# Kernel tuning notes

Hardware: AMD Instinct MI355X
Metric: run time of the kernel (lower is better)

Reference implementation:

```python
import jax, jax.numpy as jnp
import numpy as np

K = 7  # local_kernel_size


def conv2d(x, w, b, pad):
    # x: [B,C,H,W], w: [O,I,kh,kw]
    y = jax.lax.conv_general_dilated(
        x, w, window_strides=(1, 1), padding=[(pad, pad), (pad, pad)],
        dimension_numbers=("NCHW", "OIHW", "NCHW"))
    return y + b[None, :, None, None]


def kernel_normalize(kernel, k):
    # kernel: [B, k*k, H, W]; zero-mean over tap dim, then add 1/(k*k)
    km = jnp.mean(kernel, axis=1, keepdims=True)
    return kernel - km + 1.0 / (k * k)


def local_conv_feat(img, kernel, k):
    # Fused dynamic local conv: avoids materializing [B,C,k*k,H,W].
    # Tap order matches F.unfold row-major (dy, dx).
    B, C, H, W = img.shape
    pad = (k - 1) // 2
    imgp = jnp.pad(img, ((0, 0), (0, 0), (pad, pad), (pad, pad)))
    out = jnp.zeros_like(img)
    for dy in range(k):
        for dx in range(k):
            idx = dy * k + dx
            out = out + imgp[:, :, dy:dy + H, dx:dx + W] * kernel[:, idx:idx + 1]
    return out


def setup_inputs() -> dict:
    key = jax.random.key(0)
    ks = jax.random.split(key, 14)
    B, C, H, W = 4, 64, 128, 128
    w = lambda k, shape: jax.random.normal(k, shape, jnp.float32) * 0.05
    return {
        "x": jax.random.normal(ks[0], (B, C, H, W), jnp.float32),
        "kernel_features": jax.random.normal(ks[1], (B, C, H, W), jnp.float32),
        # feature_path: two 3x3 convs
        "fw1": w(ks[2], (C, C, 3, 3)), "fb1": jnp.zeros((C,), jnp.float32),
        "fw2": w(ks[3], (C, C, 3, 3)), "fb2": jnp.zeros((C,), jnp.float32),
        # multiplicative_path: two 3x3 convs
        "mw1": w(ks[4], (C, C, 3, 3)), "mb1": jnp.zeros((C,), jnp.float32),
        "mw2": w(ks[5], (C, C, 3, 3)), "mb2": jnp.zeros((C,), jnp.float32),
        # local_filter_path: two 1x1 convs, last outputs k*k channels
        "lw1": w(ks[6], (C, C, 1, 1)), "lb1": jnp.zeros((C,), jnp.float32),
        "lw2": w(ks[7], (K * K, C, 1, 1)), "lb2": jnp.zeros((K * K,), jnp.float32),
    }


def reference(x, kernel_features, fw1, fb1, fw2, fb2, mw1, mb1, mw2, mb2, lw1, lb1, lw2, lb2):
    # feature_path: ReLU -> conv3x3 -> ReLU -> conv3x3
    fp = conv2d(jax.nn.relu(conv2d(jax.nn.relu(x), fw1, fb1, 1)), fw2, fb2, 1)
    # multiplicative_path: conv3x3 -> ReLU -> conv3x3
    mp = conv2d(jax.nn.relu(conv2d(kernel_features, mw1, mb1, 1)), mw2, mb2, 1)
    # local_filter_path: conv1x1 -> ReLU -> conv1x1 (-> k*k channels)
    lp = conv2d(jax.nn.relu(conv2d(kernel_features, lw1, lb1, 0)), lw2, lb2, 0)
    lp = kernel_normalize(lp, K)
    feat = fp * mp
    filtered = local_conv_feat(feat, lp, K)
    return x + filtered
```

## Files before the change

kernel.cpp:

```cpp
#include <hip/hip_runtime.h>
#include <hip/hip_bf16.h>

#define Cc 64
#define Hc 128
#define Wc 128
#define HWc (Hc * Wc)
#define Bc 4

typedef __attribute__((ext_vector_type(8))) short short8;
typedef __attribute__((ext_vector_type(4))) float float4v;

static __device__ __forceinline__ unsigned short f2bu(float f) {
    __hip_bfloat16 h = __float2bfloat16(f);
    return *(unsigned short*)&h;
}

__global__ __launch_bounds__(256) void cvt_both_k(
    const float* __restrict__ x, const float* __restrict__ kf,
    unsigned short* __restrict__ xb, unsigned short* __restrict__ kfb)
{
    const int bid = blockIdx.x;
    const bool isx = bid < 256;
    const float* src = isx ? x : kf;
    unsigned short* dst = isx ? xb : kfb;
    const int px = (isx ? bid : bid - 256) * 256 + threadIdx.x;
    const int b  = px >> 14;
    const int hw = px & 16383;
    const float* s = src + (size_t)b * Cc * HWc + hw;
    unsigned short* d = dst + (size_t)px * Cc;

#pragma unroll
    for (int c8 = 0; c8 < 8; ++c8) {
        unsigned int pk[4];
#pragma unroll
        for (int jp = 0; jp < 4; ++jp) {
            float v0 = s[(size_t)(c8 * 8 + jp * 2 + 0) * HWc];
            float v1 = s[(size_t)(c8 * 8 + jp * 2 + 1) * HWc];
            if (isx) { v0 = fmaxf(v0, 0.f); v1 = fmaxf(v1, 0.f); }
            pk[jp] = (unsigned int)f2bu(v0) | ((unsigned int)f2bu(v1) << 16);
        }
        *(uint4*)(d + c8 * 8) = make_uint4(pk[0], pk[1], pk[2], pk[3]);
    }
}

__global__ __launch_bounds__(256) void wpack_all_k(
    const float* __restrict__ fw1, const float* __restrict__ fw2,
    const float* __restrict__ mw1, const float* __restrict__ mw2,
    const float* __restrict__ lw1, const float* __restrict__ lw2,
    unsigned short* __restrict__ wbase)
{
    const int bid = blockIdx.x;
    const int tid = threadIdx.x;
    if (bid < 72) {
        const int which = bid / 18;
        const float* w = (which == 0) ? fw1 : (which == 1) ? fw2 : (which == 2) ? mw1 : mw2;
        unsigned short* wb = wbase + (size_t)which * 36864;
        const int g = (bid % 18) * 256 + tid;
        if (g >= 4608) return;
        const int lane = g & 63;
        const int smt  = g >> 6;
        const int s    = smt >> 2;
        const int mt   = smt & 3;
        const int co   = mt * 16 + (lane & 15);
        const int kb   = s * 32 + (lane >> 4) * 8;
        unsigned int pk[4];
#pragma unroll
        for (int jp = 0; jp < 4; ++jp) {
            int k0 = kb + jp * 2, k1 = k0 + 1;
            float v0 = w[((size_t)co * Cc + (k0 & 63)) * 9 + (k0 >> 6)];
            float v1 = w[((size_t)co * Cc + (k1 & 63)) * 9 + (k1 >> 6)];
            pk[jp] = (unsigned int)f2bu(v0) | ((unsigned int)f2bu(v1) << 16);
        }
        *(uint4*)(wb + (size_t)g * 8) = make_uint4(pk[0], pk[1], pk[2], pk[3]);
    } else {
        const int which = (bid - 72) >> 1;
        const float* w = which ? lw2 : lw1;
        const int Cout = which ? 49 : 64;
        unsigned short* wb = wbase + 4 * 36864 + (size_t)which * 4096;
        const int g = ((bid - 72) & 1) * 256 + tid;
        const int lane = g & 63;
        const int smt  = g >> 6;
        const int s    = smt >> 2;
        const int mt   = smt & 3;
        const int co   = mt * 16 + (lane & 15);
        const int kb   = s * 32 + (lane >> 4) * 8;
        unsigned int pk[4];
#pragma unroll
        for (int jp = 0; jp < 4; ++jp) {
            int k0 = kb + jp * 2, k1 = k0 + 1;
            float v0 = (co < Cout) ? w[(size_t)co * Cc + k0] : 0.f;
            float v1 = (co < Cout) ? w[(size_t)co * Cc + k1] : 0.f;
            pk[jp] = (unsigned int)f2bu(v0) | ((unsigned int)f2bu(v1) << 16);
        }
        *(uint4*)(wb + (size_t)g * 8) = make_uint4(pk[0], pk[1], pk[2], pk[3]);
    }
}

template <bool RELU_OUT, bool MUL, bool F32_NCHW_OUT, bool DUAL>
__global__ __launch_bounds__(256) void conv3x3_v4(
    const unsigned short* __restrict__ in0,
    const unsigned short* __restrict__ in1,
    const unsigned short* __restrict__ wfrag0,
    const unsigned short* __restrict__ wfrag1,
    const float* __restrict__ bias0,
    const float* __restrict__ bias1,
    const unsigned short* __restrict__ fp_mul,
    void* __restrict__ out0, void* __restrict__ out1)
{
    __shared__ unsigned short s_b[264 * 64];

    const int tid  = threadIdx.x;
    const int lane = tid & 63;
    const int wv   = tid >> 6;
    const int w0   = blockIdx.x * 64;
    const int h0   = blockIdx.y * 2;
    const int zz   = blockIdx.z;
    const int b    = DUAL ? (zz & 3) : zz;
    const bool sel = DUAL ? (zz >> 2) : 0;

    const unsigned short* in    = sel ? in1 : in0;
    const unsigned short* wfrag = sel ? wfrag1 : wfrag0;
    const float*          bias  = sel ? bias1 : bias0;
    void*                 out   = sel ? out1 : out0;

    for (int u = tid; u < 264; u += 256) {
        const int r  = u / 66;
        const int c  = u - r * 66;
        const int gh = h0 - 1 + r;
        const int gw = w0 - 1 + c;
        const bool ok = ((unsigned)gh < (unsigned)Hc) && ((unsigned)gw < (unsigned)Wc);
        const unsigned short* src =
            in + (((size_t)b * Hc + (ok ? gh : 0)) * Wc + (ok ? gw : 0)) * Cc;
        const int sw = u & 7;
#pragma unroll
        for (int ch = 0; ch < 8; ++ch) {
            uint4 v = ok ? *(const uint4*)(src + ch * 8) : make_uint4(0, 0, 0, 0);
            *(uint4*)&s_b[u * 64 + ((ch ^ sw) << 3)] = v;
        }
    }
    __syncthreads();

    const int rowsel = wv >> 1;
    const int cohalf = wv & 1;
    const int quad   = lane >> 4;
    const int n15    = lane & 15;

    const unsigned short* aptr = wfrag + (((size_t)(cohalf * 2) * 64 + lane) << 3);

    int rowb[3];
#pragma unroll
    for (int ky = 0; ky < 3; ++ky) rowb[ky] = (rowsel + ky) * 66 + n15;

    float4v acc[2][4];
#pragma unroll
    for (int m = 0; m < 2; ++m)
#pragma unroll
        for (int nt = 0; nt < 4; ++nt) acc[m][nt] = (float4v){0.f, 0.f, 0.f, 0.f};

#define LOAD_A(s, m) (*(const short8*)(aptr + (size_t)(s) * 2048 + (size_t)(m) * 512))
#define LOAD_B(s, nt) ({                                                     \
        const int tap_ = (s) >> 1;                                           \
        const int qb_  = rowb[tap_ / 3] + tap_ % 3;                          \
        const int ch0_ = ((s) & 1) * 4 + quad;                               \
        *(const short8*)&s_b[(qb_ + (nt) * 16) * 64 + ((ch0_ ^ (qb_ & 7)) << 3)]; })

    short8 a_cur[2], b_cur[4];
#pragma unroll
    for (int m = 0; m < 2; ++m) a_cur[m] = LOAD_A(0, m);
#pragma unroll
    for (int nt = 0; nt < 4; ++nt) b_cur[nt] = LOAD_B(0, nt);

#pragma unroll
    for (int s = 0; s < 18; ++s) {
        short8 a_nxt[2], b_nxt[4];
        if (s < 17) {
#pragma unroll
            for (int m = 0; m < 2; ++m) a_nxt[m] = LOAD_A(s + 1, m);
#pragma unroll
            for (int nt = 0; nt < 4; ++nt) b_nxt[nt] = LOAD_B(s + 1, nt);
        }
#pragma unroll
        for (int nt = 0; nt < 4; ++nt)
#pragma unroll
            for (int m = 0; m < 2; ++m)
                acc[m][nt] = __builtin_amdgcn_mfma_f32_16x16x32_bf16(
                    a_cur[m], b_cur[nt], acc[m][nt], 0, 0, 0);
        if (s < 17) {
#pragma unroll
            for (int m = 0; m < 2; ++m) a_cur[m] = a_nxt[m];
#pragma unroll
            for (int nt = 0; nt < 4; ++nt) b_cur[nt] = b_nxt[nt];
        }
    }
#undef LOAD_A
#undef LOAD_B

    const int h = h0 + rowsel;
#pragma unroll
    for (int m = 0; m < 2; ++m) {
        const int mt  = cohalf * 2 + m;
        const int co0 = mt * 16 + quad * 4;
        float4 bv = *(const float4*)&bias[co0];
#pragma unroll
        for (int nt = 0; nt < 4; ++nt) {
            const size_t pix = ((size_t)b * Hc + h) * Wc + w0 + nt * 16 + n15;
            float v[4] = {acc[m][nt][0] + bv.x, acc[m][nt][1] + bv.y,
                          acc[m][nt][2] + bv.z, acc[m][nt][3] + bv.w};
            if (RELU_OUT)
#pragma unroll
                for (int r = 0; r < 4; ++r) v[r] = fmaxf(v[r], 0.f);
            if (MUL) {
                uint2 mm = *(const uint2*)&fp_mul[pix * Cc + co0];
                v[0] *= __uint_as_float((mm.x & 0xffffu) << 16);
                v[1] *= __uint_as_float(mm.x & 0xffff0000u);
                v[2] *= __uint_as_float((mm.y & 0xffffu) << 16);
                v[3] *= __uint_as_float(mm.y & 0xffff0000u);
            }
            if (F32_NCHW_OUT) {
                float* op = (float*)out;
#pragma unroll
                for (int r = 0; r < 4; ++r)
                    op[((size_t)b * Cc + co0 + r) * HWc + (size_t)h * Wc + w0 + nt * 16 + n15] = v[r];
            } else {
                unsigned short* op = (unsigned short*)out;
                ushort4 pk;
                pk.x = f2bu(v[0]); pk.y = f2bu(v[1]); pk.z = f2bu(v[2]); pk.w = f2bu(v[3]);
                *(ushort4*)&op[pix * Cc + co0] = pk;
            }
        }
    }
}

__global__ __launch_bounds__(256) void lp_fused_k(
    const unsigned short* __restrict__ in,
    const unsigned short* __restrict__ w1,
    const float* __restrict__ b1,
    const unsigned short* __restrict__ w2,
    const float* __restrict__ b2,
    float* __restrict__ out)
{
    __shared__ unsigned short s_t[4 * 1024];

    const int tid  = threadIdx.x;
    const int lane = tid & 63;
    const int wv   = tid >> 6;
    const int quad = lane >> 4;
    const int p    = lane & 15;
    const size_t pix = (size_t)blockIdx.x * 64 + wv * 16 + p;
    unsigned short* st = &s_t[wv * 1024];

    float4v acc1[4];
#pragma unroll
    for (int mt = 0; mt < 4; ++mt) acc1[mt] = (float4v){0.f, 0.f, 0.f, 0.f};
#pragma unroll
    for (int s = 0; s < 2; ++s) {
        short8 bfr = *(const short8*)&in[pix * Cc + s * 32 + quad * 8];
#pragma unroll
        for (int mt = 0; mt < 4; ++mt) {
            short8 afr = *(const short8*)&w1[(size_t)(((s * 4 + mt) << 6) + lane) << 3];
            acc1[mt] = __builtin_amdgcn_mfma_f32_16x16x32_bf16(afr, bfr, acc1[mt], 0, 0, 0);
        }
    }

#pragma unroll
    for (int mt = 0; mt < 4; ++mt) {
        const int co0 = mt * 16 + quad * 4;
        float4 bv = *(const float4*)&b1[co0];
        ushort4 pk;
        pk.x = f2bu(fmaxf(acc1[mt][0] + bv.x, 0.f));
        pk.y = f2bu(fmaxf(acc1[mt][1] + bv.y, 0.f));
        pk.z = f2bu(fmaxf(acc1[mt][2] + bv.z, 0.f));
        pk.w = f2bu(fmaxf(acc1[mt][3] + bv.w, 0.f));
        const int cg = co0 >> 3;
        *(ushort4*)&st[p * 64 + ((cg ^ (p & 7)) << 3) + (quad & 1) * 4] = pk;
    }
    __syncthreads();

    float4v acc2[4];
#pragma unroll
    for (int mt = 0; mt < 4; ++mt) acc2[mt] = (float4v){0.f, 0.f, 0.f, 0.f};
#pragma unroll
    for (int s = 0; s < 2; ++s) {
        const int cg = s * 4 + quad;
        short8 bfr = *(const short8*)&st[p * 64 + ((cg ^ (p & 7)) << 3)];
#pragma unroll
        for (int mt = 0; mt < 4; ++mt) {
            short8 afr = *(const short8*)&w2[(size_t)(((s * 4 + mt) << 6) + lane) << 3];
            acc2[mt] = __builtin_amdgcn_mfma_f32_16x16x32_bf16(afr, bfr, acc2[mt], 0, 0, 0);
        }
    }

    float v[4][4];
    float partial = 0.f;
#pragma unroll
    for (int mt = 0; mt < 4; ++mt) {
#pragma unroll
        for (int r = 0; r < 4; ++r) {
            const int tap = mt * 16 + quad * 4 + r;
            float val = (tap < 49) ? (acc2[mt][r] + b2[tap]) : 0.f;
            v[mt][r] = val;
            partial += val;
        }
    }
    partial += __shfl_xor(partial, 16, 64);
    partial += __shfl_xor(partial, 32, 64);
    const float m = partial * (1.f / 49.f) - (1.f / 49.f);

    const int b  = (int)(pix >> 14);
    const int hw = (int)(pix & 16383);
#pragma unroll
    for (int mt = 0; mt < 4; ++mt) {
#pragma unroll
        for (int r = 0; r < 4; ++r) {
            const int tap = mt * 16 + quad * 4 + r;
            if (tap < 49)
                out[((size_t)b * 49 + tap) * HWc + hw] = v[mt][r] - m;
        }
    }
}

__global__ __launch_bounds__(256) void local_conv_v2(
    const float* __restrict__ x, const float* __restrict__ feat,
    const float* __restrict__ lp, float* __restrict__ out)
{
    const int tid = threadIdx.x;
    const int w4  = (tid & 31) * 4;
    const int ro  = tid >> 5;
    const int h   = blockIdx.x * 8 + ro;
    const int c0  = blockIdx.y * 4;
    const int b   = blockIdx.z;

    float msk[12];
#pragma unroll
    for (int e = 0; e < 12; ++e) {
        int gw = w4 - 4 + e;
        msk[e] = ((unsigned)gw < (unsigned)Wc) ? 1.f : 0.f;
    }

    float acc[4][4];
#pragma unroll
    for (int ch = 0; ch < 4; ++ch)
#pragma unroll
        for (int p = 0; p < 4; ++p) acc[ch][p] = 0.f;

    const float* lpb = lp + (size_t)b * 49 * HWc + (size_t)h * Wc + w4;
    const float* fb  = feat + ((size_t)b * Cc + c0) * HWc;

#pragma unroll
    for (int dy = 0; dy < 7; ++dy) {
        const int gh = h + dy - 3;
        if ((unsigned)gh >= (unsigned)Hc) continue;

        float4 lp4[7];
#pragma unroll
        for (int dx = 0; dx < 7; ++dx)
            lp4[dx] = *(const float4*)&lpb[(size_t)(dy * 7 + dx) * HWc];

        const float* frow = fb + (size_t)gh * Wc + w4;
#pragma unroll
        for (int ch = 0; ch < 4; ++ch) {
            const float* fr = frow + (size_t)ch * HWc;
            float4 a  = *(const float4*)(fr - 4);
            float4 bq = *(const float4*)(fr);
            float4 cq = *(const float4*)(fr + 4);
            float f[12];
            f[0]  = a.x;            f[1]  = a.y * msk[1];
            f[2]  = a.z * msk[2];   f[3]  = a.w * msk[3];
            f[4]  = bq.x;           f[5]  = bq.y;
            f[6]  = bq.z;           f[7]  = bq.w;
            f[8]  = cq.x * msk[8];  f[9]  = cq.y * msk[9];
            f[10] = cq.z * msk[10]; f[11] = cq.w;
#pragma unroll
            for (int dx = 0; dx < 7; ++dx) {
                const float* lpv = (const float*)&lp4[dx];
#pragma unroll
                for (int p = 0; p < 4; ++p)
                    acc[ch][p] = fmaf(f[p + dx + 1], lpv[p], acc[ch][p]);
            }
        }
    }

#pragma unroll
    for (int ch = 0; ch < 4; ++ch) {
        const size_t idx = ((size_t)b * Cc + c0 + ch) * HWc + (size_t)h * Wc + w4;
        float4 xv = *(const float4*)&x[idx];
        float4 r  = {acc[ch][0] + xv.x, acc[ch][1] + xv.y,
                     acc[ch][2] + xv.z, acc[ch][3] + xv.w};
        *(float4*)&out[idx] = r;
    }
}

extern "C" void kernel_launch(void* const* d_in, const int* in_sizes, int n_in,
                              void* d_out, int out_size, void* d_ws, size_t ws_size,
                              hipStream_t stream)
{
    const float* x   = (const float*)d_in[0];
    const float* kf  = (const float*)d_in[1];
    const float* fw1 = (const float*)d_in[2];
    const float* fb1 = (const float*)d_in[3];
    const float* fw2 = (const float*)d_in[4];
    const float* fb2 = (const float*)d_in[5];
    const float* mw1 = (const float*)d_in[6];
    const float* mb1 = (const float*)d_in[7];
    const float* mw2 = (const float*)d_in[8];
    const float* mb2 = (const float*)d_in[9];
    const float* lw1 = (const float*)d_in[10];
    const float* lb1 = (const float*)d_in[11];
    const float* lw2 = (const float*)d_in[12];
    const float* lb2 = (const float*)d_in[13];

    float* out = (float*)d_out;
    char*  ws  = (char*)d_ws;

    const size_t NBH = (size_t)Bc * HWc * Cc * 2;
    const size_t NBF = (size_t)Bc * Cc * HWc * 4;
    const size_t LPB = (size_t)Bc * 49 * HWc * 4;

    unsigned short* t1f   = (unsigned short*)(ws);
    unsigned short* t1m   = (unsigned short*)(ws + NBH);
    float*          feat  = (float*)(ws + 2 * NBH);
    float*          lpb   = (float*)(ws + 2 * NBH + NBF);
    unsigned short* xb    = (unsigned short*)(ws + 2 * NBH + NBF + LPB);
    unsigned short* kfb   = (unsigned short*)((char*)xb + NBH);
    unsigned short* wbase = (unsigned short*)((char*)kfb + NBH);
    unsigned short* wb1   = wbase;
    unsigned short* wb2   = wbase + 36864;
    unsigned short* wb3   = wbase + 2 * 36864;
    unsigned short* wb4   = wbase + 3 * 36864;
    unsigned short* wl1   = wbase + 4 * 36864;
    unsigned short* wl2   = wbase + 4 * 36864 + 4096;
    unsigned short* fp    = (unsigned short*)d_out;

    dim3 blk(256);
    dim3 gm (Wc / 64, Hc / 2, Bc);
    dim3 gm2(Wc / 64, Hc / 2, Bc * 2);
    dim3 gp (Bc * HWc / 64);
    dim3 glc(Hc / 8, Cc / 4, Bc);

    cvt_both_k<<<dim3(512), blk, 0, stream>>>(x, kf, xb, kfb);
    wpack_all_k<<<dim3(76), blk, 0, stream>>>(fw1, fw2, mw1, mw2, lw1, lw2, wbase);

    conv3x3_v4<true, false, false, true><<<gm2, blk, 0, stream>>>(
        xb, kfb, wb1, wb3, fb1, mb1, nullptr, t1f, t1m);

    conv3x3_v4<false, false, false, false><<<gm, blk, 0, stream>>>(
        t1f, nullptr, wb2, nullptr, fb2, nullptr, nullptr, fp, nullptr);

    conv3x3_v4<false, true, true, false><<<gm, blk, 0, stream>>>(
        t1m, nullptr, wb4, nullptr, mb2, nullptr, fp, feat, nullptr);

    lp_fused_k<<<gp, blk, 0, stream>>>(kfb, wl1, lb1, wl2, lb2, lpb);

    local_conv_v2<<<glc, blk, 0, stream>>>(x, feat, lpb, out);
}
```

Before: 194.1 us.

## Fuse second-stage convs and fold local filter path into local conv

Merges the feature and multiplicative second 3x3 convs into one kernel that keeps the feature result in registers and multiplies before writing feat. Also computes the 1x1 local-filter path per 16x4 tile inside the local conv kernel, holding normalized taps in shared memory instead of a full fp32 buffer. This removes global round trips for fp and the 49-tap filter tensor and two launches, at the cost of fewer concurrent conv blocks and smaller local-conv tiles with more halo reloads of feat.

After: 203.0 us. 1.05x slower.

```diff
diff --git a/kernel.cpp b/kernel.cpp
--- a/kernel.cpp
+++ b/kernel.cpp
@@ -96,16 +96,70 @@
     }
 }
 
-template <bool RELU_OUT, bool MUL, bool F32_NCHW_OUT, bool DUAL>
-__global__ __launch_bounds__(256) void conv3x3_v4(
+#define STAGE_TILE(INPTR)                                                     \
+    for (int u = tid; u < 264; u += 256) {                                    \
+        const int r_  = u / 66;                                               \
+        const int c_  = u - r_ * 66;                                          \
+        const int gh_ = h0 - 1 + r_;                                          \
+        const int gw_ = w0 - 1 + c_;                                          \
+        const bool ok_ = ((unsigned)gh_ < (unsigned)Hc) && ((unsigned)gw_ < (unsigned)Wc); \
+        const unsigned short* src_ =                                          \
+            (INPTR) + (((size_t)b * Hc + (ok_ ? gh_ : 0)) * Wc + (ok_ ? gw_ : 0)) * Cc; \
+        const int sw_ = u & 7;                                                \
+        _Pragma("unroll")                                                     \
+        for (int ch_ = 0; ch_ < 8; ++ch_) {                                   \
+            uint4 v_ = ok_ ? *(const uint4*)(src_ + ch_ * 8) : make_uint4(0, 0, 0, 0); \
+            *(uint4*)&s_b[u * 64 + ((ch_ ^ sw_) << 3)] = v_;                  \
+        }                                                                     \
+    }
+
+#define LOAD_A(W, s, m) (*(const short8*)((W) + (size_t)(s) * 2048 + (size_t)(m) * 512))
+#define LOAD_B(s, nt) ({                                                      \
+        const int tap_ = (s) >> 1;                                            \
+        const int qb_  = rowb[tap_ / 3] + tap_ % 3;                           \
+        const int ch0_ = ((s) & 1) * 4 + quad;                                \
+        *(const short8*)&s_b[(qb_ + (nt) * 16) * 64 + ((ch0_ ^ (qb_ & 7)) << 3)]; })
+
+#define CONV_GEMM(APTR, ACC)                                                  \
+    {                                                                         \
+        short8 a_cur[2], b_cur[4];                                            \
+        _Pragma("unroll")                                                     \
+        for (int m = 0; m < 2; ++m) a_cur[m] = LOAD_A(APTR, 0, m);            \
+        _Pragma("unroll")                                                     \
+        for (int nt = 0; nt < 4; ++nt) b_cur[nt] = LOAD_B(0, nt);             \
+        _Pragma("unroll")                                                     \
+        for (int s = 0; s < 18; ++s) {                                        \
+            short8 a_nxt[2], b_nxt[4];                                        \
+            if (s < 17) {                                                     \
+                _Pragma("unroll")                                             \
+                for (int m = 0; m < 2; ++m) a_nxt[m] = LOAD_A(APTR, s + 1, m);\
+                _Pragma("unroll")                                             \
+                for (int nt = 0; nt < 4; ++nt) b_nxt[nt] = LOAD_B(s + 1, nt); \
+            }                                                                 \
+            _Pragma("unroll")                                                 \
+            for (int nt = 0; nt < 4; ++nt)                                    \
+                _Pragma("unroll")                                             \
+                for (int m = 0; m < 2; ++m)                                   \
+                    ACC[m][nt] = __builtin_amdgcn_mfma_f32_16x16x32_bf16(     \
+                        a_cur[m], b_cur[nt], ACC[m][nt], 0, 0, 0);            \
+            if (s < 17) {                                                     \
+                _Pragma("unroll")                                             \
+                for (int m = 0; m < 2; ++m) a_cur[m] = a_nxt[m];              \
+                _Pragma("unroll")                                             \
+                for (int nt = 0; nt < 4; ++nt) b_cur[nt] = b_nxt[nt];         \
+            }                                                                 \
+        }                                                                     \
+    }
+
+__global__ __launch_bounds__(256) void conv1_dual_k(
     const unsigned short* __restrict__ in0,
     const unsigned short* __restrict__ in1,
     const unsigned short* __restrict__ wfrag0,
     const unsigned short* __restrict__ wfrag1,
     const float* __restrict__ bias0,
     const float* __restrict__ bias1,
-    const unsigned short* __restrict__ fp_mul,
-    void* __restrict__ out0, void* __restrict__ out1)
+    unsigned short* __restrict__ out0,
+    unsigned short* __restrict__ out1)
 {
     __shared__ unsigned short s_b[264 * 64];
 
@@ -115,36 +169,21 @@
     const int w0   = blockIdx.x * 64;
     const int h0   = blockIdx.y * 2;
     const int zz   = blockIdx.z;
-    const int b    = DUAL ? (zz & 3) : zz;
-    const bool sel = DUAL ? (zz >> 2) : 0;
+    const int b    = zz & 3;
+    const bool sel = zz >> 2;
 
     const unsigned short* in    = sel ? in1 : in0;
     const unsigned short* wfrag = sel ? wfrag1 : wfrag0;
     const float*          bias  = sel ? bias1 : bias0;
-    void*                 out   = sel ? out1 : out0;
-
-    for (int u = tid; u < 264; u += 256) {
-        const int r  = u / 66;
-        const int c  = u - r * 66;
-        const int gh = h0 - 1 + r;
-        const int gw = w0 - 1 + c;
-        const bool ok = ((unsigned)gh < (unsigned)Hc) && ((unsigned)gw < (unsigned)Wc);
-        const unsigned short* src =
-            in + (((size_t)b * Hc + (ok ? gh : 0)) * Wc + (ok ? gw : 0)) * Cc;
-        const int sw = u & 7;
-#pragma unroll
-        for (int ch = 0; ch < 8; ++ch) {
-            uint4 v = ok ? *(const uint4*)(src + ch * 8) : make_uint4(0, 0, 0, 0);
-            *(uint4*)&s_b[u * 64 + ((ch ^ sw) << 3)] = v;
-        }
-    }
+    unsigned short*       out   = sel ? out1 : out0;
+
+    STAGE_TILE(in);
     __syncthreads();
 
     const int rowsel = wv >> 1;
     const int cohalf = wv & 1;
     const int quad   = lane >> 4;
     const int n15    = lane & 15;
-
     const unsigned short* aptr = wfrag + (((size_t)(cohalf * 2) * 64 + lane) << 3);
 
     int rowb[3];
@@ -157,43 +196,7 @@
 #pragma unroll
         for (int nt = 0; nt < 4; ++nt) acc[m][nt] = (float4v){0.f, 0.f, 0.f, 0.f};
 
-#define LOAD_A(s, m) (*(const short8*)(aptr + (size_t)(s) * 2048 + (size_t)(m) * 512))
-#define LOAD_B(s, nt) ({                                                     \
-        const int tap_ = (s) >> 1;                                           \
-        const int qb_  = rowb[tap_ / 3] + tap_ % 3;                          \
-        const int ch0_ = ((s) & 1) * 4 + quad;                               \
-        *(const short8*)&s_b[(qb_ + (nt) * 16) * 64 + ((ch0_ ^ (qb_ & 7)) << 3)]; })
-
-    short8 a_cur[2], b_cur[4];
-#pragma unroll
-    for (int m = 0; m < 2; ++m) a_cur[m] = LOAD_A(0, m);
-#pragma unroll
-    for (int nt = 0; nt < 4; ++nt) b_cur[nt] = LOAD_B(0, nt);
-
-#pragma unroll
-    for (int s = 0; s < 18; ++s) {
-        short8 a_nxt[2], b_nxt[4];
-        if (s < 17) {
-#pragma unroll
-            for (int m = 0; m < 2; ++m) a_nxt[m] = LOAD_A(s + 1, m);
-#pragma unroll
-            for (int nt = 0; nt < 4; ++nt) b_nxt[nt] = LOAD_B(s + 1, nt);
-        }
-#pragma unroll
-        for (int nt = 0; nt < 4; ++nt)
-#pragma unroll
-            for (int m = 0; m < 2; ++m)
-                acc[m][nt] = __builtin_amdgcn_mfma_f32_16x16x32_bf16(
-                    a_cur[m], b_cur[nt], acc[m][nt], 0, 0, 0);
-        if (s < 17) {
-#pragma unroll
-            for (int m = 0; m < 2; ++m) a_cur[m] = a_nxt[m];
-#pragma unroll
-            for (int nt = 0; nt < 4; ++nt) b_cur[nt] = b_nxt[nt];
-        }
-    }
-#undef LOAD_A
-#undef LOAD_B
+    CONV_GEMM(aptr, acc);
 
     const int h = h0 + rowsel;
 #pragma unroll
@@ -204,41 +207,116 @@
 #pragma unroll
         for (int nt = 0; nt < 4; ++nt) {
             const size_t pix = ((size_t)b * Hc + h) * Wc + w0 + nt * 16 + n15;
+            ushort4 pk;
+            pk.x = f2bu(fmaxf(acc[m][nt][0] + bv.x, 0.f));
+            pk.y = f2bu(fmaxf(acc[m][nt][1] + bv.y, 0.f));
+            pk.z = f2bu(fmaxf(acc[m][nt][2] + bv.z, 0.f));
+            pk.w = f2bu(fmaxf(acc[m][nt][3] + bv.w, 0.f));
+            *(ushort4*)&out[pix * Cc + co0] = pk;
+        }
+    }
+}
+
+__global__ __launch_bounds__(256) void conv2_fused_k(
+    const unsigned short* __restrict__ t1f,
+    const unsigned short* __restrict__ t1m,
+    const unsigned short* __restrict__ wf,
+    const unsigned short* __restrict__ wm,
+    const float* __restrict__ bf,
+    const float* __restrict__ bm,
+    float* __restrict__ feat)
+{
+    __shared__ unsigned short s_b[264 * 64];
+
+    const int tid  = threadIdx.x;
+    const int lane = tid & 63;
+    const int wv   = tid >> 6;
+    const int w0   = blockIdx.x * 64;
+    const int h0   = blockIdx.y * 2;
+    const int b    = blockIdx.z;
+
+    const int rowsel = wv >> 1;
+    const int cohalf = wv & 1;
+    const int quad   = lane >> 4;
+    const int n15    = lane & 15;
+
+    int rowb[3];
+#pragma unroll
+    for (int ky = 0; ky < 3; ++ky) rowb[ky] = (rowsel + ky) * 66 + n15;
+
+    STAGE_TILE(t1f);
+    __syncthreads();
+
+    float4v acc[2][4];
+#pragma unroll
+    for (int m = 0; m < 2; ++m)
+#pragma unroll
+        for (int nt = 0; nt < 4; ++nt) acc[m][nt] = (float4v){0.f, 0.f, 0.f, 0.f};
+
+    {
+        const unsigned short* aptr = wf + (((size_t)(cohalf * 2) * 64 + lane) << 3);
+        CONV_GEMM(aptr, acc);
+    }
+
+    unsigned int fpk[2][4][2];
+#pragma unroll
+    for (int m = 0; m < 2; ++m) {
+        const int mt  = cohalf * 2 + m;
+        const int co0 = mt * 16 + quad * 4;
+        float4 bv = *(const float4*)&bf[co0];
+#pragma unroll
+        for (int nt = 0; nt < 4; ++nt) {
+            fpk[m][nt][0] = (unsigned int)f2bu(acc[m][nt][0] + bv.x)
+                          | ((unsigned int)f2bu(acc[m][nt][1] + bv.y) << 16);
+            fpk[m][nt][1] = (unsigned int)f2bu(acc[m][nt][2] + bv.z)
+                          | ((unsigned int)f2bu(acc[m][nt][3] + bv.w) << 16);
+        }
+    }
+
+    __syncthreads();
+
+    STAGE_TILE(t1m);
+    __syncthreads();
+
+#pragma unroll
+    for (int m = 0; m < 2; ++m)
+#pragma unroll
+        for (int nt = 0; nt < 4; ++nt) acc[m][nt] = (float4v){0.f, 0.f, 0.f, 0.f};
+
+    {
+        const unsigned short* aptr = wm + (((size_t)(cohalf * 2) * 64 + lane) << 3);
+        CONV_GEMM(aptr, acc);
+    }
+
+    const int h = h0 + rowsel;
+#pragma unroll
+    for (int m = 0; m < 2; ++m) {
+        const int mt  = cohalf * 2 + m;
+        const int co0 = mt * 16 + quad * 4;
+        float4 bv = *(const float4*)&bm[co0];
+#pragma unroll
+        for (int nt = 0; nt < 4; ++nt) {
             float v[4] = {acc[m][nt][0] + bv.x, acc[m][nt][1] + bv.y,
                           acc[m][nt][2] + bv.z, acc[m][nt][3] + bv.w};
-            if (RELU_OUT)
-#pragma unroll
-                for (int r = 0; r < 4; ++r) v[r] = fmaxf(v[r], 0.f);
-            if (MUL) {
-                uint2 mm = *(const uint2*)&fp_mul[pix * Cc + co0];
-                v[0] *= __uint_as_float((mm.x & 0xffffu) << 16);
-                v[1] *= __uint_as_float(mm.x & 0xffff0000u);
-                v[2] *= __uint_as_float((mm.y & 0xffffu) << 16);
-                v[3] *= __uint_as_float(mm.y & 0xffff0000u);
-            }
-            if (F32_NCHW_OUT) {
-                float* op = (float*)out;
-#pragma unroll
-                for (int r = 0; r < 4; ++r)
-                    op[((size_t)b * Cc + co0 + r) * HWc + (size_t)h * Wc + w0 + nt * 16 + n15] = v[r];
-            } else {
-                unsigned short* op = (unsigned short*)out;
-                ushort4 pk;
-                pk.x = f2bu(v[0]); pk.y = f2bu(v[1]); pk.z = f2bu(v[2]); pk.w = f2bu(v[3]);
-                *(ushort4*)&op[pix * Cc + co0] = pk;
-            }
-        }
-    }
-}
-
-__global__ __launch_bounds__(256) void lp_fused_k(
-    const unsigned short* __restrict__ in,
-    const unsigned short* __restrict__ w1,
-    const float* __restrict__ b1,
-    const unsigned short* __restrict__ w2,
-    const float* __restrict__ b2,
+            v[0] *= __uint_as_float((fpk[m][nt][0] & 0xffffu) << 16);
+            v[1] *= __uint_as_float(fpk[m][nt][0] & 0xffff0000u);
+            v[2] *= __uint_as_float((fpk[m][nt][1] & 0xffffu) << 16);
+            v[3] *= __uint_as_float(fpk[m][nt][1] & 0xffff0000u);
+#pragma unroll
+            for (int r = 0; r < 4; ++r)
+                feat[((size_t)b * Cc + co0 + r) * HWc + (size_t)h * Wc + w0 + nt * 16 + n15] = v[r];
+        }
+    }
+}
+
+__global__ __launch_bounds__(256) void local_fused_k(
+    const unsigned short* __restrict__ kfb,
+    const unsigned short* __restrict__ w1, const float* __restrict__ b1,
+    const unsigned short* __restrict__ w2, const float* __restrict__ b2,
+    const float* __restrict__ x, const float* __restrict__ feat,
     float* __restrict__ out)
 {
+    __shared__ float s_lp[49][68];
     __shared__ unsigned short s_t[4 * 1024];
 
     const int tid  = threadIdx.x;
@@ -246,94 +324,94 @@
     const int wv   = tid >> 6;
     const int quad = lane >> 4;
     const int p    = lane & 15;
-    const size_t pix = (size_t)blockIdx.x * 64 + wv * 16 + p;
-    unsigned short* st = &s_t[wv * 1024];
-
-    float4v acc1[4];
-#pragma unroll
-    for (int mt = 0; mt < 4; ++mt) acc1[mt] = (float4v){0.f, 0.f, 0.f, 0.f};
-#pragma unroll
-    for (int s = 0; s < 2; ++s) {
-        short8 bfr = *(const short8*)&in[pix * Cc + s * 32 + quad * 8];
+    const int w0   = blockIdx.x * 16;
+    const int h0   = blockIdx.y * 4;
+    const int b    = blockIdx.z;
+
+    {
+        const size_t pix = ((size_t)b * Hc + h0 + wv) * Wc + w0 + p;
+        unsigned short* st = &s_t[wv * 1024];
+
+        float4v acc1[4];
+#pragma unroll
+        for (int mt = 0; mt < 4; ++mt) acc1[mt] = (float4v){0.f, 0.f, 0.f, 0.f};
+#pragma unroll
+        for (int s = 0; s < 2; ++s) {
+            short8 bfr = *(const short8*)&kfb[pix * Cc + s * 32 + quad * 8];
+#pragma unroll
+            for (int mt = 0; mt < 4; ++mt) {
+                short8 afr = *(const short8*)&w1[(size_t)(((s * 4 + mt) << 6) + lane) << 3];
+                acc1[mt] = __builtin_amdgcn_mfma_f32_16x16x32_bf16(afr, bfr, acc1[mt], 0, 0, 0);
+            }
+        }
+
 #pragma unroll
         for (int mt = 0; mt < 4; ++mt) {
-            short8 afr = *(const short8*)&w1[(size_t)(((s * 4 + mt) << 6) + lane) << 3];
-            acc1[mt] = __builtin_amdgcn_mfma_f32_16x16x32_bf16(afr, bfr, acc1[mt], 0, 0, 0);
-        }
-    }
-
-#pragma unroll
-    for (int mt = 0; mt < 4; ++mt) {
-        const int co0 = mt * 16 + quad * 4;
-        float4 bv = *(const float4*)&b1[co0];
-        ushort4 pk;
-        pk.x = f2bu(fmaxf(acc1[mt][0] + bv.x, 0.f));
-        pk.y = f2bu(fmaxf(acc1[mt][1] + bv.y, 0.f));
-        pk.z = f2bu(fmaxf(acc1[mt][2] + bv.z, 0.f));
-        pk.w = f2bu(fmaxf(acc1[mt][3] + bv.w, 0.f));
-        const int cg = co0 >> 3;
-        *(ushort4*)&st[p * 64 + ((cg ^ (p & 7)) << 3) + (quad & 1) * 4] = pk;
+            const int co0 = mt * 16 + quad * 4;
+            float4 bv = *(const float4*)&b1[co0];
+            ushort4 pk;
+            pk.x = f2bu(fmaxf(acc1[mt][0] + bv.x, 0.f));
+            pk.y = f2bu(fmaxf(acc1[mt][1] + bv.y, 0.f));
+            pk.z = f2bu(fmaxf(acc1[mt][2] + bv.z, 0.f));
+            pk.w = f2bu(fmaxf(acc1[mt][3] + bv.w, 0.f));
+            const int cg = co0 >> 3;
+            *(ushort4*)&st[p * 64 + ((cg ^ (p & 7)) << 3) + (quad & 1) * 4] = pk;
+        }
+        __syncthreads();
+
+        float4v acc2[4];
+#pragma unroll
+        for (int mt = 0; mt < 4; ++mt) acc2[mt] = (float4v){0.f, 0.f, 0.f, 0.f};
+#pragma unroll
+        for (int s = 0; s < 2; ++s) {
+            const int cg = s * 4 + quad;
+            short8 bfr = *(const short8*)&st[p * 64 + ((cg ^ (p & 7)) << 3)];
+#pragma unroll
+            for (int mt = 0; mt < 4; ++mt) {
+                short8 afr = *(const short8*)&w2[(size_t)(((s * 4 + mt) << 6) + lane) << 3];
+                acc2[mt] = __builtin_amdgcn_mfma_f32_16x16x32_bf16(afr, bfr, acc2[mt], 0, 0, 0);
+            }
+        }
+
+        float v[4][4];
+        float partial = 0.f;
+#pragma unroll
+        for (int mt = 0; mt < 4; ++mt) {
+#pragma unroll
+            for (int r = 0; r < 4; ++r) {
+                const int tap = mt * 16 + quad * 4 + r;
+                float val = (tap < 49) ? (acc2[mt][r] + b2[tap]) : 0.f;
+                v[mt][r] = val;
+                partial += val;
+            }
+        }
+        partial += __shfl_xor(partial, 16, 64);
+        partial += __shfl_xor(partial, 32, 64);
+        const float mmean = partial * (1.f / 49.f) - (1.f / 49.f);
+
+#pragma unroll
+        for (int mt = 0; mt < 4; ++mt) {
+#pragma unroll
+            for (int r = 0; r < 4; ++r) {
+                const int tap = mt * 16 + quad * 4 + r;
+                if (tap < 49) s_lp[tap][wv * 16 + p] = v[mt][r] - mmean;
+            }
+        }
     }
     __syncthreads();
 
-    float4v acc2[4];
-#pragma unroll
-    for (int mt = 0; mt < 4; ++mt) acc2[mt] = (float4v){0.f, 0.f, 0.f, 0.f};
-#pragma unroll
-    for (int s = 0; s < 2; ++s) {
-        const int cg = s * 4 + quad;
-        short8 bfr = *(const short8*)&st[p * 64 + ((cg ^ (p & 7)) << 3)];
-#pragma unroll
-        for (int mt = 0; mt < 4; ++mt) {
-            short8 afr = *(const short8*)&w2[(size_t)(((s * 4 + mt) << 6) + lane) << 3];
-            acc2[mt] = __builtin_amdgcn_mfma_f32_16x16x32_bf16(afr, bfr, acc2[mt], 0, 0, 0);
-        }
-    }
-
-    float v[4][4];
-    float partial = 0.f;
-#pragma unroll
-    for (int mt = 0; mt < 4; ++mt) {
-#pragma unroll
-        for (int r = 0; r < 4; ++r) {
-            const int tap = mt * 16 + quad * 4 + r;
-            float val = (tap < 49) ? (acc2[mt][r] + b2[tap]) : 0.f;
-            v[mt][r] = val;
-            partial += val;
-        }
-    }
-    partial += __shfl_xor(partial, 16, 64);
-    partial += __shfl_xor(partial, 32, 64);
-    const float m = partial * (1.f / 49.f) - (1.f / 49.f);
-
-    const int b  = (int)(pix >> 14);
-    const int hw = (int)(pix & 16383);
-#pragma unroll
-    for (int mt = 0; mt < 4; ++mt) {
-#pragma unroll
-        for (int r = 0; r < 4; ++r) {
-            const int tap = mt * 16 + quad * 4 + r;
-            if (tap < 49)
-                out[((size_t)b * 49 + tap) * HWc + hw] = v[mt][r] - m;
-        }
-    }
-}
-
-__global__ __launch_bounds__(256) void local_conv_v2(
-    const float* __restrict__ x, const float* __restrict__ feat,
-    const float* __restrict__ lp, float* __restrict__ out)
-{
-    const int tid = threadIdx.x;
-    const int w4  = (tid & 31) * 4;
-    const int ro  = tid >> 5;
-    const int h   = blockIdx.x * 8 + ro;
-    const int c0  = blockIdx.y * 4;
-    const int b   = blockIdx.z;
+    const int cg2 = tid >> 4;
+    const int pg  = tid & 15;
+    const int r2  = pg >> 2;
+    const int c4  = (pg & 3) * 4;
+    const int c0  = cg2 * 4;
+    const int h   = h0 + r2;
+    const int w4g = w0 + c4;
 
     float msk[12];
 #pragma unroll
     for (int e = 0; e < 12; ++e) {
-        int gw = w4 - 4 + e;
+        int gw = w4g - 4 + e;
         msk[e] = ((unsigned)gw < (unsigned)Wc) ? 1.f : 0.f;
     }
 
@@ -341,10 +419,9 @@
 #pragma unroll
     for (int ch = 0; ch < 4; ++ch)
 #pragma unroll
-        for (int p = 0; p < 4; ++p) acc[ch][p] = 0.f;
-
-    const float* lpb = lp + (size_t)b * 49 * HWc + (size_t)h * Wc + w4;
-    const float* fb  = feat + ((size_t)b * Cc + c0) * HWc;
+        for (int pq = 0; pq < 4; ++pq) acc[ch][pq] = 0.f;
+
+    const float* fb = feat + ((size_t)b * Cc + c0) * HWc;
 
 #pragma unroll
     for (int dy = 0; dy < 7; ++dy) {
@@ -354,9 +431,9 @@
         float4 lp4[7];
 #pragma unroll
         for (int dx = 0; dx < 7; ++dx)
-            lp4[dx] = *(const float4*)&lpb[(size_t)(dy * 7 + dx) * HWc];
-
-        const float* frow = fb + (size_t)gh * Wc + w4;
+            lp4[dx] = *(const float4*)&s_lp[dy * 7 + dx][r2 * 16 + c4];
+
+        const float* frow = fb + (size_t)gh * Wc + w4g;
 #pragma unroll
         for (int ch = 0; ch < 4; ++ch) {
             const float* fr = frow + (size_t)ch * HWc;
@@ -374,15 +451,15 @@
             for (int dx = 0; dx < 7; ++dx) {
                 const float* lpv = (const float*)&lp4[dx];
 #pragma unroll
-                for (int p = 0; p < 4; ++p)
-                    acc[ch][p] = fmaf(f[p + dx + 1], lpv[p], acc[ch][p]);
+                for (int pq = 0; pq < 4; ++pq)
+                    acc[ch][pq] = fmaf(f[pq + dx + 1], lpv[pq], acc[ch][pq]);
             }
         }
     }
 
 #pragma unroll
     for (int ch = 0; ch < 4; ++ch) {
-        const size_t idx = ((size_t)b * Cc + c0 + ch) * HWc + (size_t)h * Wc + w4;
+        const size_t idx = ((size_t)b * Cc + c0 + ch) * HWc + (size_t)h * Wc + w4g;
         float4 xv = *(const float4*)&x[idx];
         float4 r  = {acc[ch][0] + xv.x, acc[ch][1] + xv.y,
                      acc[ch][2] + xv.z, acc[ch][3] + xv.w};
@@ -414,13 +491,11 @@
 
     const size_t NBH = (size_t)Bc * HWc * Cc * 2;
     const size_t NBF = (size_t)Bc * Cc * HWc * 4;
-    const size_t LPB = (size_t)Bc * 49 * HWc * 4;
 
     unsigned short* t1f   = (unsigned short*)(ws);
     unsigned short* t1m   = (unsigned short*)(ws + NBH);
     float*          feat  = (float*)(ws + 2 * NBH);
-    float*          lpb   = (float*)(ws + 2 * NBH + NBF);
-    unsigned short* xb    = (unsigned short*)(ws + 2 * NBH + NBF + LPB);
+    unsigned short* xb    = (unsigned short*)(ws + 2 * NBH + NBF);
     unsigned short* kfb   = (unsigned short*)((char*)xb + NBH);
     unsigned short* wbase = (unsigned short*)((char*)kfb + NBH);
     unsigned short* wb1   = wbase;
@@ -429,27 +504,18 @@
     unsigned short* wb4   = wbase + 3 * 36864;
     unsigned short* wl1   = wbase + 4 * 36864;
     unsigned short* wl2   = wbase + 4 * 36864 + 4096;
-    unsigned short* fp    = (unsigned short*)d_out;
 
     dim3 blk(256);
+    dim3 gm2(Wc / 64, Hc / 2, Bc * 2);
     dim3 gm (Wc / 64, Hc / 2, Bc);
-    dim3 gm2(Wc / 64, Hc / 2, Bc * 2);
-    dim3 gp (Bc * HWc / 64);
-    dim3 glc(Hc / 8, Cc / 4, Bc);
+    dim3 glf(Wc / 16, Hc / 4, Bc);
 
     cvt_both_k<<<dim3(512), blk, 0, stream>>>(x, kf, xb, kfb);
     wpack_all_k<<<dim3(76), blk, 0, stream>>>(fw1, fw2, mw1, mw2, lw1, lw2, wbase);
 
-    conv3x3_v4<true, false, false, true><<<gm2, blk, 0, stream>>>(
-        xb, kfb, wb1, wb3, fb1, mb1, nullptr, t1f, t1m);
-
-    conv3x3_v4<false, false, false, false><<<gm, blk, 0, stream>>>(
-        t1f, nullptr, wb2, nullptr, fb2, nullptr, nullptr, fp, nullptr);
-
-    conv3x3_v4<false, true, true, false><<<gm, blk, 0, stream>>>(
-        t1m, nullptr, wb4, nullptr, mb2, nullptr, fp, feat, nullptr);
-
-    lp_fused_k<<<gp, blk, 0, stream>>>(kfb, wl1, lb1, wl2, lb2, lpb);
-
-    local_conv_v2<<<glc, blk, 0, stream>>>(x, feat, lpb, out);
-}
+    conv1_dual_k<<<gm2, blk, 0, stream>>>(xb, kfb, wb1, wb3, fb1, mb1, t1f, t1m);
+
+    conv2_fused_k<<<gm, blk, 0, stream>>>(t1f, t1m, wb2, wb4, fb2, mb2, feat);
+
+    local_fused_k<<<glf, blk, 0, stream>>>(kfb, wl1, lb1, wl2, lb2, x, feat, out);
+}
```
